# Performance work log

Measured on AMD Instinct MI355X. Metric: run time of the kernel, lower is better.

## Reference

```python
import jax, jax.numpy as jnp
import numpy as np

B, S, H = 4, 2048, 2048


def _rotate_half(x):
    x1, x2 = jnp.split(x, 2, axis=-1)
    return jnp.concatenate((-x2, x1), axis=-1)


def _rope_tables(seq_len, dim, dtype):
    # standard RoPE over the full hidden dim (emb last dim == dim so it
    # broadcasts against [B,S,dim] activations)
    inv_freq = 1.0 / (10000.0 ** (jnp.arange(0, dim, 2, dtype=jnp.float32) / dim))
    t = jnp.arange(seq_len, dtype=jnp.float32)
    freqs = jnp.einsum('s,d->sd', t, inv_freq)          # [S, dim/2]
    emb = jnp.concatenate((freqs, freqs), axis=-1)      # [S, dim]
    return jnp.cos(emb).astype(dtype)[None], jnp.sin(emb).astype(dtype)[None]  # [1,S,dim]


def setup_inputs() -> dict:
    key = jax.random.key(0)
    ks = jax.random.split(key, 11)
    sc = 0.02
    return {
        'query': jax.random.normal(ks[0], (B, S, H), jnp.float32),
        'key':   jax.random.normal(ks[1], (B, S, H), jnp.float32),
        'value': jax.random.normal(ks[2], (B, S, H), jnp.float32),
        'Wq': jax.random.normal(ks[3], (H, H), jnp.float32) * sc,
        'bq': jax.random.normal(ks[4], (H,), jnp.float32) * sc,
        'Wk': jax.random.normal(ks[5], (H, H), jnp.float32) * sc,
        'bk': jax.random.normal(ks[6], (H,), jnp.float32) * sc,
        'Wv': jax.random.normal(ks[7], (H, H), jnp.float32) * sc,
        'bv': jax.random.normal(ks[8], (H,), jnp.float32) * sc,
        'Wo': jax.random.normal(ks[9], (H, H), jnp.float32) * sc,
        'bo': jax.random.normal(ks[10], (H,), jnp.float32) * sc,
    }


def reference(query, key, value, Wq, bq, Wk, bk, Wv, bv, Wo, bo):
    seq, dim = query.shape[1], query.shape[2]
    cos, sin = _rope_tables(seq, dim, query.dtype)      # [1,S,H]
    q_rot = query * cos + _rotate_half(query) * sin     # RoPE BEFORE projections
    k_rot = key * cos + _rotate_half(key) * sin
    q = jnp.einsum('bsh,oh->bso', q_rot, Wq) + bq       # torch Linear: x @ W.T + b
    k = jnp.einsum('bsh,oh->bso', k_rot, Wk) + bk
    v = jnp.einsum('bsh,oh->bso', value, Wv) + bv
    scale = 1.0 / jnp.sqrt(jnp.asarray(dim, q.dtype))
    scores = jnp.einsum('bqh,bkh->bqk', q, k) * scale   # [B,Sq,Sk]
    probs = jax.nn.softmax(scores, axis=-1)
    context = jnp.einsum('bqk,bkh->bqh', probs, v)
    return jnp.einsum('bsh,oh->bso', context, Wo) + bo
```

## Files before the change

### kernel.cpp

```cpp
#include <hip/hip_runtime.h>


typedef __bf16 bf16_t;
typedef bf16_t bf16x8 __attribute__((ext_vector_type(8)));
typedef bf16_t bf16x4 __attribute__((ext_vector_type(4)));
typedef float  f32x4  __attribute__((ext_vector_type(4)));

#define BDIM 4
#define SDIM 2048
#define HDIM 2048

__device__ __forceinline__ void async_copy16(const bf16_t* g, bf16_t* l) {
  __builtin_amdgcn_global_load_lds(
      (__attribute__((address_space(1))) const void*)g,
      (__attribute__((address_space(3))) void*)l,
      16, 0, 0);
}

__global__ __launch_bounds__(256) void rope_kernel(
    const float* __restrict__ q, const float* __restrict__ k,
    bf16_t* __restrict__ qr, bf16_t* __restrict__ kr) {
  const int i = blockIdx.x * 256 + threadIdx.x;
  const int j = i & 1023;
  const int row = i >> 10;
  const int s = row & (SDIM - 1);
  const float invf = exp2f(-(float)j * 0.012976281620653759f);
  const float f = (float)s * invf;
  float sn, cs;
  sincosf(f, &sn, &cs);
  const long base = (long)row * HDIM;
  const float q1 = q[base + j], q2 = q[base + j + 1024];
  const float k1 = k[base + j], k2 = k[base + j + 1024];
  qr[base + j]        = (bf16_t)(q1 * cs - q2 * sn);
  qr[base + j + 1024] = (bf16_t)(q2 * cs + q1 * sn);
  kr[base + j]        = (bf16_t)(k1 * cs - k2 * sn);
  kr[base + j + 1024] = (bf16_t)(k2 * cs + k1 * sn);
}

__global__ __launch_bounds__(256) void cast_kernel(
    const float* __restrict__ src, bf16_t* __restrict__ dst, int n4) {
  const int i = blockIdx.x * 256 + threadIdx.x;
  if (i >= n4) return;
  const float4 v = ((const float4*)src)[i];
  bf16x4 o;
  o[0] = (bf16_t)v.x; o[1] = (bf16_t)v.y; o[2] = (bf16_t)v.z; o[3] = (bf16_t)v.w;
  *(bf16x4*)&dst[(long)i * 4] = o;
}

template <bool OUTF32>
__global__ __launch_bounds__(256, 2) void gemm_bt(
    const bf16_t* __restrict__ A, const bf16_t* __restrict__ Bt,
    void* __restrict__ Cv, const float* __restrict__ bias,
    int M, int N, int K, float alpha,
    long sA, long sB, long sC) {
  __shared__ __align__(16) bf16_t As[128 * 64];
  __shared__ __align__(16) bf16_t Bs[128 * 64];
  const int z = blockIdx.z;
  A  += (long)z * sA;
  Bt += (long)z * sB;
  const int tid  = threadIdx.x;
  const int lane = tid & 63;
  const int wave = tid >> 6;
  const int wm = (wave >> 1) * 64;
  const int wn = (wave & 1) * 64;
  const int m0 = blockIdx.y * 128;
  const int n0 = blockIdx.x * 128;
  const int lrow = lane & 15;
  const int quad = lane >> 4;
  const int swz  = lrow & 7;

  f32x4 acc[4][4] = {};

  const long aBase = (long)m0 * K;
  const long bBase = (long)n0 * K;

  const int rl  = lane >> 3;
  const int ccs = ((lane & 7) ^ rl) * 8;

  for (int k0 = 0; k0 < K; k0 += 64) {
#pragma unroll
    for (int i = 0; i < 4; ++i) {
      const int c = wave * 4 + i;
      const int r = c * 8 + rl;
      async_copy16(A  + aBase + (long)r * K + k0 + ccs, As + c * 512);
      async_copy16(Bt + bBase + (long)r * K + k0 + ccs, Bs + c * 512);
    }
    __syncthreads();
#pragma unroll
    for (int ks = 0; ks < 64; ks += 32) {
      bf16x8 af[4], bfr[4];
      const int cg = (ks >> 3) + quad;
      const int j  = (cg ^ swz) * 8;
#pragma unroll
      for (int t = 0; t < 4; ++t)
        af[t] = *(const bf16x8*)&As[(wm + t * 16 + lrow) * 64 + j];
#pragma unroll
      for (int t = 0; t < 4; ++t)
        bfr[t] = *(const bf16x8*)&Bs[(wn + t * 16 + lrow) * 64 + j];
#pragma unroll
      for (int mt = 0; mt < 4; ++mt)
#pragma unroll
        for (int nt = 0; nt < 4; ++nt)
          acc[mt][nt] = __builtin_amdgcn_mfma_f32_16x16x32_bf16(
              af[mt], bfr[nt], acc[mt][nt], 0, 0, 0);
    }
    __syncthreads();
  }

#pragma unroll
  for (int mt = 0; mt < 4; ++mt) {
#pragma unroll
    for (int nt = 0; nt < 4; ++nt) {
      const int col = n0 + wn + nt * 16 + lrow;
      const float bv = bias ? bias[col] : 0.0f;
#pragma unroll
      for (int r = 0; r < 4; ++r) {
        const int row = m0 + wm + mt * 16 + quad * 4 + r;
        const float v = acc[mt][nt][r] * alpha + bv;
        if (OUTF32)
          ((float*)Cv)[(long)z * sC + (long)row * N + col] = v;
        else
          ((bf16_t*)Cv)[(long)z * sC + (long)row * N + col] = (bf16_t)v;
      }
    }
  }
}

__global__ __launch_bounds__(256) void softmax_kernel(
    const float* __restrict__ Sc, bf16_t* __restrict__ P) {
  const long row = blockIdx.x;
  const float* src = Sc + row * SDIM;
  bf16_t* dst = P + row * SDIM;
  const int tid = threadIdx.x;
  float4 a = ((const float4*)src)[tid];
  float4 b = ((const float4*)src)[tid + 256];
  float m = fmaxf(fmaxf(fmaxf(a.x, a.y), fmaxf(a.z, a.w)),
                  fmaxf(fmaxf(b.x, b.y), fmaxf(b.z, b.w)));
#pragma unroll
  for (int off = 32; off; off >>= 1) m = fmaxf(m, __shfl_xor(m, off));
  __shared__ float redm[4], reds[4];
  const int wave = tid >> 6, lane = tid & 63;
  if (lane == 0) redm[wave] = m;
  __syncthreads();
  m = fmaxf(fmaxf(redm[0], redm[1]), fmaxf(redm[2], redm[3]));
  a.x = __expf(a.x - m); a.y = __expf(a.y - m);
  a.z = __expf(a.z - m); a.w = __expf(a.w - m);
  b.x = __expf(b.x - m); b.y = __expf(b.y - m);
  b.z = __expf(b.z - m); b.w = __expf(b.w - m);
  float s = a.x + a.y + a.z + a.w + b.x + b.y + b.z + b.w;
#pragma unroll
  for (int off = 32; off; off >>= 1) s += __shfl_xor(s, off);
  if (lane == 0) reds[wave] = s;
  __syncthreads();
  s = reds[0] + reds[1] + reds[2] + reds[3];
  const float inv = 1.0f / s;
  bf16x4 o0, o1;
  o0[0] = (bf16_t)(a.x * inv); o0[1] = (bf16_t)(a.y * inv);
  o0[2] = (bf16_t)(a.z * inv); o0[3] = (bf16_t)(a.w * inv);
  o1[0] = (bf16_t)(b.x * inv); o1[1] = (bf16_t)(b.y * inv);
  o1[2] = (bf16_t)(b.z * inv); o1[3] = (bf16_t)(b.w * inv);
  *(bf16x4*)&dst[tid * 4] = o0;
  *(bf16x4*)&dst[1024 + tid * 4] = o1;
}

__global__ __launch_bounds__(256) void transpose_bf16(
    const bf16_t* __restrict__ in, bf16_t* __restrict__ out, int rows, int cols) {
  __shared__ bf16_t tile[64][72];
  const long bo = (long)blockIdx.z * rows * cols;
  in += bo; out += bo;
  const int c0 = blockIdx.x * 64, r0 = blockIdx.y * 64;
  const int t = threadIdx.x;
  const int lr = t >> 3;
  const int lc = (t & 7) * 8;
#pragma unroll
  for (int i = 0; i < 2; ++i) {
    const int r = lr + i * 32;
    bf16x8 v = *(const bf16x8*)&in[(long)(r0 + r) * cols + c0 + lc];
    *(bf16x8*)&tile[r][lc] = v;
  }
  __syncthreads();
#pragma unroll
  for (int i = 0; i < 2; ++i) {
    const int r = lr + i * 32;
    bf16x8 v;
#pragma unroll
    for (int j = 0; j < 8; ++j) v[j] = tile[lc + j][r];
    *(bf16x8*)&out[(long)(c0 + r) * rows + r0 + lc] = v;
  }
}

extern "C" void kernel_launch(void* const* d_in, const int* in_sizes, int n_in,
                              void* d_out, int out_size, void* d_ws, size_t ws_size,
                              hipStream_t stream) {
  const float* q_in = (const float*)d_in[0];
  const float* k_in = (const float*)d_in[1];
  const float* v_in = (const float*)d_in[2];
  const float* Wq = (const float*)d_in[3];
  const float* bq = (const float*)d_in[4];
  const float* Wk = (const float*)d_in[5];
  const float* bk = (const float*)d_in[6];
  const float* Wv = (const float*)d_in[7];
  const float* bv = (const float*)d_in[8];
  const float* Wo = (const float*)d_in[9];
  const float* bo = (const float*)d_in[10];
  float* out = (float*)d_out;

  const size_t ELE  = (size_t)BDIM * SDIM * HDIM;
  const size_t WELE = (size_t)HDIM * HDIM;
  const size_t SEG  = ELE * 2;

  uint8_t* w = (uint8_t*)d_ws;
  bf16_t* qr  = (bf16_t*)(w + 0 * SEG);
  bf16_t* kr  = (bf16_t*)(w + 1 * SEG);
  bf16_t* vb  = (bf16_t*)(w + 2 * SEG);
  bf16_t* Wb  = (bf16_t*)(w + 3 * SEG);
  bf16_t* qp  = (bf16_t*)(w + 4 * SEG);
  bf16_t* kp  = (bf16_t*)(w + 5 * SEG);
  bf16_t* vp  = (bf16_t*)(w + 6 * SEG);
  float*  scores = (float*)(w + 0 * SEG);
  bf16_t* probs  = (bf16_t*)(w + 2 * SEG);
  bf16_t* vpT    = (bf16_t*)(w + 4 * SEG);
  bf16_t* ctx    = (bf16_t*)(w + 5 * SEG);

  bf16_t* Wqb = Wb + 0 * WELE;
  bf16_t* Wkb = Wb + 1 * WELE;
  bf16_t* Wvb = Wb + 2 * WELE;
  bf16_t* Wob = Wb + 3 * WELE;

  const dim3 blk(256);
  const long SH = (long)SDIM * HDIM;
  const long SS = (long)SDIM * SDIM;

  rope_kernel<<<dim3(ELE / 2 / 256), blk, 0, stream>>>(q_in, k_in, qr, kr);
  cast_kernel<<<dim3(ELE / 4 / 256), blk, 0, stream>>>(v_in, vb, (int)(ELE / 4));
  cast_kernel<<<dim3(WELE / 4 / 256), blk, 0, stream>>>(Wq, Wqb, (int)(WELE / 4));
  cast_kernel<<<dim3(WELE / 4 / 256), blk, 0, stream>>>(Wk, Wkb, (int)(WELE / 4));
  cast_kernel<<<dim3(WELE / 4 / 256), blk, 0, stream>>>(Wv, Wvb, (int)(WELE / 4));
  cast_kernel<<<dim3(WELE / 4 / 256), blk, 0, stream>>>(Wo, Wob, (int)(WELE / 4));
  gemm_bt<false><<<dim3(16, 64, 1), blk, 0, stream>>>(qr, Wqb, qp, bq,
      BDIM * SDIM, HDIM, HDIM, 1.0f, 0, 0, 0);
  gemm_bt<false><<<dim3(16, 64, 1), blk, 0, stream>>>(kr, Wkb, kp, bk,
      BDIM * SDIM, HDIM, HDIM, 1.0f, 0, 0, 0);
  gemm_bt<false><<<dim3(16, 64, 1), blk, 0, stream>>>(vb, Wvb, vp, bv,
      BDIM * SDIM, HDIM, HDIM, 1.0f, 0, 0, 0);
  gemm_bt<true><<<dim3(16, 16, BDIM), blk, 0, stream>>>(qp, kp, scores, nullptr,
      SDIM, SDIM, HDIM, 0.022097086912079612f, SH, SH, SS);
  softmax_kernel<<<dim3(BDIM * SDIM), blk, 0, stream>>>(scores, probs);
  transpose_bf16<<<dim3(32, 32, BDIM), blk, 0, stream>>>(vp, vpT, SDIM, HDIM);
  gemm_bt<false><<<dim3(16, 16, BDIM), blk, 0, stream>>>(probs, vpT, ctx, nullptr,
      SDIM, HDIM, SDIM, 1.0f, SS, SH, SH);
  gemm_bt<true><<<dim3(16, 64, 1), blk, 0, stream>>>(ctx, Wob, out, bo,
      BDIM * SDIM, HDIM, HDIM, 1.0f, 0, 0, 0);
}
```

Baseline: 761.5 us.

## Fuse prep casts, write V projection transposed, store scores in bf16

The V cast moves into the RoPE kernel, and the four weight casts are merged into one launch. The V projection GEMM now writes its output transposed, which removes the separate transpose kernel. Attention scores are stored as bf16 instead of fp32, halving score traffic through softmax. The risks are lost precision in the pre-softmax scores and strided 8-byte stores in the transposed epilogue.

```diff
diff --git a/kernel.cpp b/kernel.cpp
--- a/kernel.cpp
+++ b/kernel.cpp
@@ -17,9 +17,10 @@
       16, 0, 0);
 }
 
-__global__ __launch_bounds__(256) void rope_kernel(
+__global__ __launch_bounds__(256) void prep_kernel(
     const float* __restrict__ q, const float* __restrict__ k,
-    bf16_t* __restrict__ qr, bf16_t* __restrict__ kr) {
+    const float* __restrict__ v,
+    bf16_t* __restrict__ qr, bf16_t* __restrict__ kr, bf16_t* __restrict__ vb) {
   const int i = blockIdx.x * 256 + threadIdx.x;
   const int j = i & 1023;
   const int row = i >> 10;
@@ -35,19 +36,26 @@
   qr[base + j + 1024] = (bf16_t)(q2 * cs + q1 * sn);
   kr[base + j]        = (bf16_t)(k1 * cs - k2 * sn);
   kr[base + j + 1024] = (bf16_t)(k2 * cs + k1 * sn);
-}
-
-__global__ __launch_bounds__(256) void cast_kernel(
-    const float* __restrict__ src, bf16_t* __restrict__ dst, int n4) {
-  const int i = blockIdx.x * 256 + threadIdx.x;
-  if (i >= n4) return;
-  const float4 v = ((const float4*)src)[i];
-  bf16x4 o;
-  o[0] = (bf16_t)v.x; o[1] = (bf16_t)v.y; o[2] = (bf16_t)v.z; o[3] = (bf16_t)v.w;
-  *(bf16x4*)&dst[(long)i * 4] = o;
-}
-
-template <bool OUTF32>
+  vb[base + j]        = (bf16_t)v[base + j];
+  vb[base + j + 1024] = (bf16_t)v[base + j + 1024];
+}
+
+__global__ __launch_bounds__(256) void wcast_kernel(
+    const float* __restrict__ w0, const float* __restrict__ w1,
+    const float* __restrict__ w2, const float* __restrict__ w3,
+    bf16_t* __restrict__ dst) {
+  const int wsel = blockIdx.y;
+  const float* src = wsel == 0 ? w0 : wsel == 1 ? w1 : wsel == 2 ? w2 : w3;
+  const long i = (long)(blockIdx.x * 256 + threadIdx.x) * 8;
+  const float4 a = *(const float4*)&src[i];
+  const float4 b = *(const float4*)&src[i + 4];
+  bf16x8 o;
+  o[0] = (bf16_t)a.x; o[1] = (bf16_t)a.y; o[2] = (bf16_t)a.z; o[3] = (bf16_t)a.w;
+  o[4] = (bf16_t)b.x; o[5] = (bf16_t)b.y; o[6] = (bf16_t)b.z; o[7] = (bf16_t)b.w;
+  *(bf16x8*)&dst[(long)wsel * HDIM * HDIM + i] = o;
+}
+
+template <int OMODE>
 __global__ __launch_bounds__(256, 2) void gemm_bt(
     const bf16_t* __restrict__ A, const bf16_t* __restrict__ Bt,
     void* __restrict__ Cv, const float* __restrict__ bias,
@@ -113,29 +121,42 @@
     for (int nt = 0; nt < 4; ++nt) {
       const int col = n0 + wn + nt * 16 + lrow;
       const float bv = bias ? bias[col] : 0.0f;
-#pragma unroll
-      for (int r = 0; r < 4; ++r) {
-        const int row = m0 + wm + mt * 16 + quad * 4 + r;
-        const float v = acc[mt][nt][r] * alpha + bv;
-        if (OUTF32)
-          ((float*)Cv)[(long)z * sC + (long)row * N + col] = v;
-        else
-          ((bf16_t*)Cv)[(long)z * sC + (long)row * N + col] = (bf16_t)v;
+      if (OMODE == 2) {
+        const int row0 = m0 + wm + mt * 16 + quad * 4;
+        const int b = row0 >> 11;
+        const int s = row0 & (SDIM - 1);
+        bf16x4 o;
+#pragma unroll
+        for (int r = 0; r < 4; ++r) o[r] = (bf16_t)(acc[mt][nt][r] + bv);
+        *(bf16x4*)&((bf16_t*)Cv)[(long)b * SDIM * HDIM + (long)col * SDIM + s] = o;
+      } else {
+#pragma unroll
+        for (int r = 0; r < 4; ++r) {
+          const int row = m0 + wm + mt * 16 + quad * 4 + r;
+          const float v = acc[mt][nt][r] * alpha + bv;
+          if (OMODE == 1)
+            ((float*)Cv)[(long)z * sC + (long)row * N + col] = v;
+          else
+            ((bf16_t*)Cv)[(long)z * sC + (long)row * N + col] = (bf16_t)v;
+        }
       }
     }
   }
 }
 
 __global__ __launch_bounds__(256) void softmax_kernel(
-    const float* __restrict__ Sc, bf16_t* __restrict__ P) {
+    const bf16_t* __restrict__ Sc, bf16_t* __restrict__ P) {
   const long row = blockIdx.x;
-  const float* src = Sc + row * SDIM;
+  const bf16_t* src = Sc + row * SDIM;
   bf16_t* dst = P + row * SDIM;
   const int tid = threadIdx.x;
-  float4 a = ((const float4*)src)[tid];
-  float4 b = ((const float4*)src)[tid + 256];
-  float m = fmaxf(fmaxf(fmaxf(a.x, a.y), fmaxf(a.z, a.w)),
-                  fmaxf(fmaxf(b.x, b.y), fmaxf(b.z, b.w)));
+  const bf16x8 in = *(const bf16x8*)&src[tid * 8];
+  float x[8];
+#pragma unroll
+  for (int t = 0; t < 8; ++t) x[t] = (float)in[t];
+  float m = x[0];
+#pragma unroll
+  for (int t = 1; t < 8; ++t) m = fmaxf(m, x[t]);
 #pragma unroll
   for (int off = 32; off; off >>= 1) m = fmaxf(m, __shfl_xor(m, off));
   __shared__ float redm[4], reds[4];
@@ -143,50 +164,19 @@
   if (lane == 0) redm[wave] = m;
   __syncthreads();
   m = fmaxf(fmaxf(redm[0], redm[1]), fmaxf(redm[2], redm[3]));
-  a.x = __expf(a.x - m); a.y = __expf(a.y - m);
-  a.z = __expf(a.z - m); a.w = __expf(a.w - m);
-  b.x = __expf(b.x - m); b.y = __expf(b.y - m);
-  b.z = __expf(b.z - m); b.w = __expf(b.w - m);
-  float s = a.x + a.y + a.z + a.w + b.x + b.y + b.z + b.w;
+  float s = 0.0f;
+#pragma unroll
+  for (int t = 0; t < 8; ++t) { x[t] = __expf(x[t] - m); s += x[t]; }
 #pragma unroll
   for (int off = 32; off; off >>= 1) s += __shfl_xor(s, off);
   if (lane == 0) reds[wave] = s;
   __syncthreads();
   s = reds[0] + reds[1] + reds[2] + reds[3];
   const float inv = 1.0f / s;
-  bf16x4 o0, o1;
-  o0[0] = (bf16_t)(a.x * inv); o0[1] = (bf16_t)(a.y * inv);
-  o0[2] = (bf16_t)(a.z * inv); o0[3] = (bf16_t)(a.w * inv);
-  o1[0] = (bf16_t)(b.x * inv); o1[1] = (bf16_t)(b.y * inv);
-  o1[2] = (bf16_t)(b.z * inv); o1[3] = (bf16_t)(b.w * inv);
-  *(bf16x4*)&dst[tid * 4] = o0;
-  *(bf16x4*)&dst[1024 + tid * 4] = o1;
-}
-
-__global__ __launch_bounds__(256) void transpose_bf16(
-    const bf16_t* __restrict__ in, bf16_t* __restrict__ out, int rows, int cols) {
-  __shared__ bf16_t tile[64][72];
-  const long bo = (long)blockIdx.z * rows * cols;
-  in += bo; out += bo;
-  const int c0 = blockIdx.x * 64, r0 = blockIdx.y * 64;
-  const int t = threadIdx.x;
-  const int lr = t >> 3;
-  const int lc = (t & 7) * 8;
-#pragma unroll
-  for (int i = 0; i < 2; ++i) {
-    const int r = lr + i * 32;
-    bf16x8 v = *(const bf16x8*)&in[(long)(r0 + r) * cols + c0 + lc];
-    *(bf16x8*)&tile[r][lc] = v;
-  }
-  __syncthreads();
-#pragma unroll
-  for (int i = 0; i < 2; ++i) {
-    const int r = lr + i * 32;
-    bf16x8 v;
-#pragma unroll
-    for (int j = 0; j < 8; ++j) v[j] = tile[lc + j][r];
-    *(bf16x8*)&out[(long)(c0 + r) * rows + r0 + lc] = v;
-  }
+  bf16x8 o;
+#pragma unroll
+  for (int t = 0; t < 8; ++t) o[t] = (bf16_t)(x[t] * inv);
+  *(bf16x8*)&dst[tid * 8] = o;
 }
 
 extern "C" void kernel_launch(void* const* d_in, const int* in_sizes, int n_in,
@@ -216,11 +206,10 @@
   bf16_t* Wb  = (bf16_t*)(w + 3 * SEG);
   bf16_t* qp  = (bf16_t*)(w + 4 * SEG);
   bf16_t* kp  = (bf16_t*)(w + 5 * SEG);
-  bf16_t* vp  = (bf16_t*)(w + 6 * SEG);
-  float*  scores = (float*)(w + 0 * SEG);
+  bf16_t* vpT = (bf16_t*)(w + 6 * SEG);
+  bf16_t* scores = (bf16_t*)(w + 0 * SEG);
   bf16_t* probs  = (bf16_t*)(w + 2 * SEG);
-  bf16_t* vpT    = (bf16_t*)(w + 4 * SEG);
-  bf16_t* ctx    = (bf16_t*)(w + 5 * SEG);
+  bf16_t* ctx    = (bf16_t*)(w + 1 * SEG);
 
   bf16_t* Wqb = Wb + 0 * WELE;
   bf16_t* Wkb = Wb + 1 * WELE;
@@ -231,24 +220,19 @@
   const long SH = (long)SDIM * HDIM;
   const long SS = (long)SDIM * SDIM;
 
-  rope_kernel<<<dim3(ELE / 2 / 256), blk, 0, stream>>>(q_in, k_in, qr, kr);
-  cast_kernel<<<dim3(ELE / 4 / 256), blk, 0, stream>>>(v_in, vb, (int)(ELE / 4));
-  cast_kernel<<<dim3(WELE / 4 / 256), blk, 0, stream>>>(Wq, Wqb, (int)(WELE / 4));
-  cast_kernel<<<dim3(WELE / 4 / 256), blk, 0, stream>>>(Wk, Wkb, (int)(WELE / 4));
-  cast_kernel<<<dim3(WELE / 4 / 256), blk, 0, stream>>>(Wv, Wvb, (int)(WELE / 4));
-  cast_kernel<<<dim3(WELE / 4 / 256), blk, 0, stream>>>(Wo, Wob, (int)(WELE / 4));
-  gemm_bt<false><<<dim3(16, 64, 1), blk, 0, stream>>>(qr, Wqb, qp, bq,
-      BDIM * SDIM, HDIM, HDIM, 1.0f, 0, 0, 0);
-  gemm_bt<false><<<dim3(16, 64, 1), blk, 0, stream>>>(kr, Wkb, kp, bk,
-      BDIM * SDIM, HDIM, HDIM, 1.0f, 0, 0, 0);
-  gemm_bt<false><<<dim3(16, 64, 1), blk, 0, stream>>>(vb, Wvb, vp, bv,
-      BDIM * SDIM, HDIM, HDIM, 1.0f, 0, 0, 0);
-  gemm_bt<true><<<dim3(16, 16, BDIM), blk, 0, stream>>>(qp, kp, scores, nullptr,
+  prep_kernel<<<dim3(ELE / 2 / 256), blk, 0, stream>>>(q_in, k_in, v_in, qr, kr, vb);
+  wcast_kernel<<<dim3(WELE / 8 / 256, 4), blk, 0, stream>>>(Wq, Wk, Wv, Wo, Wb);
+  gemm_bt<0><<<dim3(16, 64, 1), blk, 0, stream>>>(qr, Wqb, qp, bq,
+      BDIM * SDIM, HDIM, HDIM, 1.0f, 0, 0, 0);
+  gemm_bt<0><<<dim3(16, 64, 1), blk, 0, stream>>>(kr, Wkb, kp, bk,
+      BDIM * SDIM, HDIM, HDIM, 1.0f, 0, 0, 0);
+  gemm_bt<2><<<dim3(16, 64, 1), blk, 0, stream>>>(vb, Wvb, vpT, bv,
+      BDIM * SDIM, HDIM, HDIM, 1.0f, 0, 0, 0);
+  gemm_bt<0><<<dim3(16, 16, BDIM), blk, 0, stream>>>(qp, kp, scores, nullptr,
       SDIM, SDIM, HDIM, 0.022097086912079612f, SH, SH, SS);
   softmax_kernel<<<dim3(BDIM * SDIM), blk, 0, stream>>>(scores, probs);
-  transpose_bf16<<<dim3(32, 32, BDIM), blk, 0, stream>>>(vp, vpT, SDIM, HDIM);
-  gemm_bt<false><<<dim3(16, 16, BDIM), blk, 0, stream>>>(probs, vpT, ctx, nullptr,
+  gemm_bt<0><<<dim3(16, 16, BDIM), blk, 0, stream>>>(probs, vpT, ctx, nullptr,
       SDIM, HDIM, SDIM, 1.0f, SS, SH, SH);
-  gemm_bt<true><<<dim3(16, 64, 1), blk, 0, stream>>>(ctx, Wob, out, bo,
-      BDIM * SDIM, HDIM, HDIM, 1.0f, 0, 0, 0);
-}
+  gemm_bt<1><<<dim3(16, 64, 1), blk, 0, stream>>>(ctx, Wob, out, bo,
+      BDIM * SDIM, HDIM, HDIM, 1.0f, 0, 0, 0);
+}
```

After: 709.3 us. -6.9%, faster.
